# Optimization experiments

Measured on AMD Instinct MI355X. Metric: run time of the kernel, lower is better.

The kernel has to match this reference:

```python
import jax, jax.numpy as jnp
import numpy as np

N = 4096      # total_activities_num
D = 128       # feature dim
E = 1_000_000 # number of edges (events)
EPS = 1e-12


def setup_inputs() -> dict:
    key = jax.random.key(0)
    k1, k2, k3, k4, k5 = jax.random.split(key, 5)
    currents = jax.random.randint(k1, (E,), 0, N, dtype=jnp.int64)
    targets = jax.random.randint(k2, (E,), 0, N, dtype=jnp.int64)
    activities_features = jax.random.normal(k3, (N, D), dtype=jnp.float32)
    cases_features = jax.random.normal(k4, (E, D), dtype=jnp.float32)
    # Learned parameter W [N, N], kaiming_uniform fan_in relu -> U(-b, b), b = sqrt(6/fan_in)
    bound = float(np.sqrt(6.0 / N))
    W = jax.random.uniform(k5, (N, N), dtype=jnp.float32, minval=-bound, maxval=bound)
    return {
        "currents": currents,
        "targets": targets,
        "activities_features": activities_features,
        "cases_features": cases_features,
        "W": W,
    }


def reference(currents, targets, activities_features, cases_features, W):
    # Per-edge gather: h_emb, t_emb are [E, D]
    h_emb = activities_features[currents]
    t_emb = activities_features[targets]
    # dist = ||h + case - t||_2 per edge -> [E]
    diff = h_emb + cases_features - t_emb
    dist = jnp.sqrt(jnp.sum(diff * diff, axis=1))
    vals = jnp.exp(-dist)
    # Scatter-add into dense [N, N] attention input at (tail, head)
    att_input = jnp.zeros((N, N), dtype=activities_features.dtype)
    att_input = att_input.at[targets, currents].add(vals)
    # Row-normalize
    norm = jnp.sum(att_input, axis=1, keepdims=True)
    attention = att_input / (norm + EPS)
    # Dense GEMMs
    feat = W @ activities_features           # [N, D]
    h = attention @ feat + feat               # [N, D]
    return h
```

## Files before the change

kernel.cpp:

```cpp
#include <hip/hip_runtime.h>
#include <hip/hip_bf16.h>

typedef unsigned short u16;
typedef unsigned int   u32;

typedef __attribute__((ext_vector_type(8))) __bf16 bf16x8;
typedef __attribute__((ext_vector_type(4))) float  f32x4;
typedef __attribute__((ext_vector_type(4))) u32    u32x4;

#define NN 4096
#define DD 128
#define EPS 1e-12f

#define KS 4
#define BM 32
#define BK 128
#define KPER (NN / KS)
#define LDK 136

static __device__ __forceinline__ u16 f2bf(float f) {
    union { float f; u32 u; } v; v.f = f;
    u32 r = v.u + 0x7fffu + ((v.u >> 16) & 1u);
    return (u16)(r >> 16);
}
static __device__ __forceinline__ float bf2f(u16 u) {
    union { u32 i; float f; } v; v.i = (u32)u << 16; return v.f;
}

template <typename T>
static __device__ __forceinline__ auto bf2_atomic_add(T* p, T v, int)
    -> decltype(unsafeAtomicAdd(p, v), void()) {
    unsafeAtomicAdd(p, v);
}
template <typename T>
static __device__ __forceinline__ void bf2_atomic_add(T* p, T v, long) {
    u32* w = (u32*)p;
    union { u32 i; T h; } av; av.h = v;
    float alo = bf2f((u16)(av.i & 0xffff));
    float ahi = bf2f((u16)(av.i >> 16));
    u32 old = *w, assumed;
    do {
        assumed = old;
        float lo = bf2f((u16)(assumed & 0xffff)) + alo;
        float hi = bf2f((u16)(assumed >> 16)) + ahi;
        u32 nv = (u32)f2bf(lo) | ((u32)f2bf(hi) << 16);
        old = atomicCAS(w, assumed, nv);
    } while (old != assumed);
}

__global__ __launch_bounds__(256) void edge_kernel(
    const int* __restrict__ currents, const int* __restrict__ targets,
    const float* __restrict__ A, const float* __restrict__ cases,
    u16* __restrict__ att, int E)
{
    int e = blockIdx.x * 8 + (threadIdx.x >> 5);
    if (e >= E) return;
    int l = threadIdx.x & 31;
    int c = currents[e];
    int t = targets[e];
    f32x4 h = *(const f32x4*)(A + (size_t)c * DD + l * 4);
    f32x4 g = *(const f32x4*)(A + (size_t)t * DD + l * 4);
    f32x4 q = __builtin_nontemporal_load((const f32x4*)(cases + (size_t)e * DD + l * 4));
    float d0 = h.x + q.x - g.x;
    float d1 = h.y + q.y - g.y;
    float d2 = h.z + q.z - g.z;
    float d3 = h.w + q.w - g.w;
    float s = d0 * d0 + d1 * d1 + d2 * d2 + d3 * d3;
#pragma unroll
    for (int m = 16; m; m >>= 1) s += __shfl_xor(s, m, 64);
    if (l == 0) {
        float val = __expf(-__fsqrt_rn(s));
        u16 b = f2bf(val);
        size_t off = (size_t)t * NN + c;
        union { u32 i; __hip_bfloat162 h2; } pk;
        pk.i = (c & 1) ? ((u32)b << 16) : (u32)b;
        bf2_atomic_add((__hip_bfloat162*)(att + (off & ~(size_t)1)), pk.h2, 0);
    }
}

__global__ __launch_bounds__(256) void transpose_to_bf16(
    const float* __restrict__ in, u16* __restrict__ out)
{
    __shared__ __align__(16) u16 lds[128][40];
    const int k0 = blockIdx.x * 32;
    const int t = threadIdx.x;
#pragma unroll
    for (int i = 0; i < 4; ++i) {
        int f  = t + 256 * i;
        int kr = f >> 5;
        int n0 = (f & 31) * 4;
        float4 v = *(const float4*)(in + (size_t)(k0 + kr) * DD + n0);
        lds[n0 + 0][kr] = f2bf(v.x);
        lds[n0 + 1][kr] = f2bf(v.y);
        lds[n0 + 2][kr] = f2bf(v.z);
        lds[n0 + 3][kr] = f2bf(v.w);
    }
    __syncthreads();
    int n = t >> 1, h = t & 1;
    uint4 v0 = *(const uint4*)&lds[n][h * 16];
    uint4 v1 = *(const uint4*)&lds[n][h * 16 + 8];
    *(uint4*)(out + (size_t)n * NN + k0 + h * 16)     = v0;
    *(uint4*)(out + (size_t)n * NN + k0 + h * 16 + 8) = v1;
}

template<bool ROWSUM, bool ABF16>
__global__ __launch_bounds__(512, 4) void gemm_splitk(
    const void* __restrict__ AmatV,
    const u16*  __restrict__ BT,
    float* __restrict__ part,
    float* __restrict__ normsum)
{
    __shared__ __align__(16) u16 As[BM * LDK];
    __shared__ __align__(16) u16 Bs[DD * LDK];

    const int m0   = blockIdx.x * BM;
    const int ks   = blockIdx.y;
    const int kbeg = ks * KPER;
    const int t    = threadIdx.x;
    const int wave = t >> 6;
    const int lane = t & 63;
    const int quad = lane >> 4;
    const int l16  = lane & 15;

    const int ar = t >> 4;
    const int aq = t & 15;
    const int bn = t >> 2;
    const int bq = t & 3;

    const float* Apf = (const float*)AmatV + (size_t)(m0 + ar) * NN + kbeg + aq * 4;
    const u16*   Aph = (const u16*)AmatV   + (size_t)(m0 + ar) * NN + kbeg + aq * 8;
    const u16*   Bp  = BT + (size_t)bn * NN + kbeg + bq * 32;

    f32x4 va0, va1; u32x4 vah;
    if constexpr (ABF16) {
        vah = __builtin_nontemporal_load((const u32x4*)Aph);
    } else {
        va0 = __builtin_nontemporal_load((const f32x4*)Apf);
        va1 = __builtin_nontemporal_load((const f32x4*)(Apf + 64));
    }
    uint4 vb0 = *(const uint4*)(Bp);
    uint4 vb1 = *(const uint4*)(Bp + 8);
    uint4 vb2 = *(const uint4*)(Bp + 16);
    uint4 vb3 = *(const uint4*)(Bp + 24);

    f32x4 acc0 = {0.f, 0.f, 0.f, 0.f};
    f32x4 acc1 = {0.f, 0.f, 0.f, 0.f};
    float rsum = 0.f;

    for (int kk = 0; kk < KPER; kk += BK) {
        if constexpr (ABF16) {
            if (ROWSUM) {
#pragma unroll
            for (int j = 0; j < 4; ++j) {
                u32 w = vah[j];
                rsum += bf2f((u16)(w & 0xffff)) + bf2f((u16)(w >> 16));
            }
            }
            *(u32x4*)&As[ar * LDK + aq * 8] = vah;
        } else {
            if (ROWSUM) {
                rsum += (va0.x + va0.y) + (va0.z + va0.w)
                      + (va1.x + va1.y) + (va1.z + va1.w);
            }
            ushort4 u0, u1;
            u0.x = f2bf(va0.x); u0.y = f2bf(va0.y); u0.z = f2bf(va0.z); u0.w = f2bf(va0.w);
            u1.x = f2bf(va1.x); u1.y = f2bf(va1.y); u1.z = f2bf(va1.z); u1.w = f2bf(va1.w);
            *(ushort4*)&As[ar * LDK + aq * 4]      = u0;
            *(ushort4*)&As[ar * LDK + aq * 4 + 64] = u1;
        }
        *(uint4*)&Bs[bn * LDK + bq * 32]      = vb0;
        *(uint4*)&Bs[bn * LDK + bq * 32 + 8]  = vb1;
        *(uint4*)&Bs[bn * LDK + bq * 32 + 16] = vb2;
        *(uint4*)&Bs[bn * LDK + bq * 32 + 24] = vb3;
        __syncthreads();

        if (kk + BK < KPER) {
            int k1 = kk + BK;
            if constexpr (ABF16) {
                vah = __builtin_nontemporal_load((const u32x4*)(Aph + k1));
            } else {
                va0 = __builtin_nontemporal_load((const f32x4*)(Apf + k1));
                va1 = __builtin_nontemporal_load((const f32x4*)(Apf + k1 + 64));
            }
            vb0 = *(const uint4*)(Bp + k1);
            vb1 = *(const uint4*)(Bp + k1 + 8);
            vb2 = *(const uint4*)(Bp + k1 + 16);
            vb3 = *(const uint4*)(Bp + k1 + 24);
        }

#pragma unroll
        for (int k2 = 0; k2 < 4; ++k2) {
            bf16x8 a0 = *(const bf16x8*)&As[l16 * LDK + k2 * 32 + quad * 8];
            bf16x8 a1 = *(const bf16x8*)&As[(16 + l16) * LDK + k2 * 32 + quad * 8];
            bf16x8 b  = *(const bf16x8*)&Bs[(wave * 16 + l16) * LDK + k2 * 32 + quad * 8];
            acc0 = __builtin_amdgcn_mfma_f32_16x16x32_bf16(a0, b, acc0, 0, 0, 0);
            acc1 = __builtin_amdgcn_mfma_f32_16x16x32_bf16(a1, b, acc1, 0, 0, 0);
        }
        __syncthreads();
    }

    float* P = part + (size_t)ks * NN * DD;
#pragma unroll
    for (int r = 0; r < 4; ++r) {
        int row0 = m0 + quad * 4 + r;
        int col  = wave * 16 + l16;
        P[(size_t)row0 * DD + col]        = acc0[r];
        P[(size_t)(row0 + 16) * DD + col] = acc1[r];
    }

    if (ROWSUM) {
#pragma unroll
        for (int m = 8; m; m >>= 1) rsum += __shfl_xor(rsum, m, 64);
        if ((t & 15) == 0) atomicAdd(normsum + m0 + ar, rsum);
    }
}

__global__ __launch_bounds__(256) void combine_feat(
    const float* __restrict__ part, float* __restrict__ feat)
{
    int i = blockIdx.x * 256 + threadIdx.x;
    const float4* p = (const float4*)part;
    const int S = NN * DD / 4;
    float4 a = p[i], b = p[i + S], c = p[i + 2 * S], d = p[i + 3 * S];
    float4 s;
    s.x = (a.x + b.x) + (c.x + d.x);
    s.y = (a.y + b.y) + (c.y + d.y);
    s.z = (a.z + b.z) + (c.z + d.z);
    s.w = (a.w + b.w) + (c.w + d.w);
    ((float4*)feat)[i] = s;
}

__global__ __launch_bounds__(256) void combine_out(
    const float* __restrict__ part, const float* __restrict__ normsum,
    const float* __restrict__ feat, float* __restrict__ out)
{
    int i = blockIdx.x * 256 + threadIdx.x;
    int row = i >> 5;
    const float4* p = (const float4*)part;
    const int S = NN * DD / 4;
    float4 a = p[i], b = p[i + S], c = p[i + 2 * S], d = p[i + 3 * S];
    float sc = 1.0f / (normsum[row] + EPS);
    float4 f = ((const float4*)feat)[i];
    float4 s;
    s.x = ((a.x + b.x) + (c.x + d.x)) * sc + f.x;
    s.y = ((a.y + b.y) + (c.y + d.y)) * sc + f.y;
    s.z = ((a.z + b.z) + (c.z + d.z)) * sc + f.z;
    s.w = ((a.w + b.w) + (c.w + d.w)) * sc + f.w;
    ((float4*)out)[i] = s;
}

extern "C" void kernel_launch(void* const* d_in, const int* in_sizes, int n_in,
                              void* d_out, int out_size, void* d_ws, size_t ws_size,
                              hipStream_t stream)
{
    const int*   currents = (const int*)d_in[0];
    const int*   targets  = (const int*)d_in[1];
    const float* acts     = (const float*)d_in[2];
    const float* cases    = (const float*)d_in[3];
    const float* W        = (const float*)d_in[4];
    float*       out      = (float*)d_out;
    const int E = in_sizes[0];

    char* ws = (char*)d_ws;
    u16*   att     = (u16*)ws;
    float* part    = (float*)(ws + (size_t)NN * NN * 2);
    float* feat    = part + (size_t)KS * NN * DD;
    u16*   BT1     = (u16*)(feat + (size_t)NN * DD);
    u16*   BT2     = BT1 + (size_t)DD * NN;
    float* normsum = (float*)(BT2 + (size_t)DD * NN);

    hipMemsetAsync(att, 0, (size_t)NN * NN * 2, stream);
    hipMemsetAsync(normsum, 0, (size_t)NN * 4, stream);

    transpose_to_bf16<<<128, 256, 0, stream>>>(acts, BT1);

    edge_kernel<<<(E + 7) / 8, 256, 0, stream>>>(currents, targets, acts, cases,
                                                 att, E);

    gemm_splitk<false, false><<<dim3(NN / BM, KS), 512, 0, stream>>>(W, BT1, part, nullptr);
    combine_feat<<<NN * DD / 4 / 256, 256, 0, stream>>>(part, feat);

    transpose_to_bf16<<<128, 256, 0, stream>>>(feat, BT2);

    gemm_splitk<true, true><<<dim3(NN / BM, KS), 512, 0, stream>>>(att, BT2, part, normsum);
    combine_out<<<NN * DD / 4 / 256, 256, 0, stream>>>(part, normsum, feat, out);
}
```

Before: 197.5 us.

## Fuse edge scatter and W@A GEMM into one heterogeneous launch

Merges the edge scatter kernel and the first split-K GEMM (W @ activities) into a single kernel. The first 512 blocks do the GEMM and the remaining blocks process edges, 16 per 512-thread block. Because the two stages are independent, this lets the compute-bound GEMM overlap the memory- and atomic-bound edge work and saves one launch. The cost is that the edge blocks inherit the GEMM's LDS footprint and launch bounds, which may reduce their occupancy.

```diff
diff --git a/kernel.cpp b/kernel.cpp
--- a/kernel.cpp
+++ b/kernel.cpp
@@ -17,6 +17,7 @@
 #define BK 128
 #define KPER (NN / KS)
 #define LDK 136
+#define NGEMM (128 * KS)
 
 static __device__ __forceinline__ u16 f2bf(float f) {
     union { float f; u32 u; } v; v.f = f;
@@ -48,33 +49,109 @@
     } while (old != assumed);
 }
 
-__global__ __launch_bounds__(256) void edge_kernel(
-    const int* __restrict__ currents, const int* __restrict__ targets,
-    const float* __restrict__ A, const float* __restrict__ cases,
-    u16* __restrict__ att, int E)
-{
-    int e = blockIdx.x * 8 + (threadIdx.x >> 5);
-    if (e >= E) return;
-    int l = threadIdx.x & 31;
-    int c = currents[e];
-    int t = targets[e];
-    f32x4 h = *(const f32x4*)(A + (size_t)c * DD + l * 4);
-    f32x4 g = *(const f32x4*)(A + (size_t)t * DD + l * 4);
-    f32x4 q = __builtin_nontemporal_load((const f32x4*)(cases + (size_t)e * DD + l * 4));
-    float d0 = h.x + q.x - g.x;
-    float d1 = h.y + q.y - g.y;
-    float d2 = h.z + q.z - g.z;
-    float d3 = h.w + q.w - g.w;
-    float s = d0 * d0 + d1 * d1 + d2 * d2 + d3 * d3;
-#pragma unroll
-    for (int m = 16; m; m >>= 1) s += __shfl_xor(s, m, 64);
-    if (l == 0) {
-        float val = __expf(-__fsqrt_rn(s));
-        u16 b = f2bf(val);
-        size_t off = (size_t)t * NN + c;
-        union { u32 i; __hip_bfloat162 h2; } pk;
-        pk.i = (c & 1) ? ((u32)b << 16) : (u32)b;
-        bf2_atomic_add((__hip_bfloat162*)(att + (off & ~(size_t)1)), pk.h2, 0);
+__global__ __launch_bounds__(512, 4) void fused_edge_gemm(
+    const int*   __restrict__ currents, const int* __restrict__ targets,
+    const float* __restrict__ A,        const float* __restrict__ cases,
+    u16*         __restrict__ att,
+    const float* __restrict__ W,        const u16* __restrict__ BT,
+    float*       __restrict__ part,     int E)
+{
+    __shared__ __align__(16) u16 As[BM * LDK];
+    __shared__ __align__(16) u16 Bs[DD * LDK];
+    const int bid = blockIdx.x;
+
+    if (bid >= NGEMM) {
+        const int e = (bid - NGEMM) * 16 + ((int)threadIdx.x >> 5);
+        if (e >= E) return;
+        const int l = threadIdx.x & 31;
+        const int c = currents[e];
+        const int t = targets[e];
+        f32x4 h = *(const f32x4*)(A + (size_t)c * DD + l * 4);
+        f32x4 g = *(const f32x4*)(A + (size_t)t * DD + l * 4);
+        f32x4 q = __builtin_nontemporal_load(
+                      (const f32x4*)(cases + (size_t)e * DD + l * 4));
+        f32x4 d = h + q - g;
+        float s = d.x * d.x + d.y * d.y + d.z * d.z + d.w * d.w;
+#pragma unroll
+        for (int m = 16; m; m >>= 1) s += __shfl_xor(s, m, 64);
+        if (l == 0) {
+            float val = __expf(-__fsqrt_rn(s));
+            u16 b = f2bf(val);
+            size_t off = (size_t)t * NN + c;
+            union { u32 i; __hip_bfloat162 h2; } pk;
+            pk.i = (c & 1) ? ((u32)b << 16) : (u32)b;
+            bf2_atomic_add((__hip_bfloat162*)(att + (off & ~(size_t)1)), pk.h2, 0);
+        }
+        return;
+    }
+
+    const int m0   = (bid & 127) * BM;
+    const int ks   = bid >> 7;
+    const int kbeg = ks * KPER;
+    const int t    = threadIdx.x;
+    const int wave = t >> 6;
+    const int lane = t & 63;
+    const int quad = lane >> 4;
+    const int l16  = lane & 15;
+
+    const int ar = t >> 4;
+    const int aq = t & 15;
+    const int bn = t >> 2;
+    const int bq = t & 3;
+
+    const float* Ap = W  + (size_t)(m0 + ar) * NN + kbeg + aq * 4;
+    const u16*   Bp = BT + (size_t)bn * NN + kbeg + bq * 32;
+
+    f32x4 va0 = __builtin_nontemporal_load((const f32x4*)Ap);
+    f32x4 va1 = __builtin_nontemporal_load((const f32x4*)(Ap + 64));
+    uint4 vb0 = *(const uint4*)(Bp);
+    uint4 vb1 = *(const uint4*)(Bp + 8);
+    uint4 vb2 = *(const uint4*)(Bp + 16);
+    uint4 vb3 = *(const uint4*)(Bp + 24);
+
+    f32x4 acc0 = {0.f, 0.f, 0.f, 0.f};
+    f32x4 acc1 = {0.f, 0.f, 0.f, 0.f};
+
+    for (int kk = 0; kk < KPER; kk += BK) {
+        ushort4 u0, u1;
+        u0.x = f2bf(va0.x); u0.y = f2bf(va0.y); u0.z = f2bf(va0.z); u0.w = f2bf(va0.w);
+        u1.x = f2bf(va1.x); u1.y = f2bf(va1.y); u1.z = f2bf(va1.z); u1.w = f2bf(va1.w);
+        *(ushort4*)&As[ar * LDK + aq * 4]      = u0;
+        *(ushort4*)&As[ar * LDK + aq * 4 + 64] = u1;
+        *(uint4*)&Bs[bn * LDK + bq * 32]      = vb0;
+        *(uint4*)&Bs[bn * LDK + bq * 32 + 8]  = vb1;
+        *(uint4*)&Bs[bn * LDK + bq * 32 + 16] = vb2;
+        *(uint4*)&Bs[bn * LDK + bq * 32 + 24] = vb3;
+        __syncthreads();
+
+        if (kk + BK < KPER) {
+            int k1 = kk + BK;
+            va0 = __builtin_nontemporal_load((const f32x4*)(Ap + k1));
+            va1 = __builtin_nontemporal_load((const f32x4*)(Ap + k1 + 64));
+            vb0 = *(const uint4*)(Bp + k1);
+            vb1 = *(const uint4*)(Bp + k1 + 8);
+            vb2 = *(const uint4*)(Bp + k1 + 16);
+            vb3 = *(const uint4*)(Bp + k1 + 24);
+        }
+
+#pragma unroll
+        for (int k2 = 0; k2 < 4; ++k2) {
+            bf16x8 a0 = *(const bf16x8*)&As[l16 * LDK + k2 * 32 + quad * 8];
+            bf16x8 a1 = *(const bf16x8*)&As[(16 + l16) * LDK + k2 * 32 + quad * 8];
+            bf16x8 b  = *(const bf16x8*)&Bs[(wave * 16 + l16) * LDK + k2 * 32 + quad * 8];
+            acc0 = __builtin_amdgcn_mfma_f32_16x16x32_bf16(a0, b, acc0, 0, 0, 0);
+            acc1 = __builtin_amdgcn_mfma_f32_16x16x32_bf16(a1, b, acc1, 0, 0, 0);
+        }
+        __syncthreads();
+    }
+
+    float* P = part + (size_t)ks * NN * DD;
+#pragma unroll
+    for (int r = 0; r < 4; ++r) {
+        int row0 = m0 + quad * 4 + r;
+        int col  = wave * 16 + l16;
+        P[(size_t)row0 * DD + col]        = acc0[r];
+        P[(size_t)(row0 + 16) * DD + col] = acc1[r];
     }
 }
 
@@ -103,9 +180,8 @@
     *(uint4*)(out + (size_t)n * NN + k0 + h * 16 + 8) = v1;
 }
 
-template<bool ROWSUM, bool ABF16>
-__global__ __launch_bounds__(512, 4) void gemm_splitk(
-    const void* __restrict__ AmatV,
+__global__ __launch_bounds__(512, 4) void gemm2_att(
+    const u16*  __restrict__ Amat,
     const u16*  __restrict__ BT,
     float* __restrict__ part,
     float* __restrict__ normsum)
@@ -127,17 +203,10 @@
     const int bn = t >> 2;
     const int bq = t & 3;
 
-    const float* Apf = (const float*)AmatV + (size_t)(m0 + ar) * NN + kbeg + aq * 4;
-    const u16*   Aph = (const u16*)AmatV   + (size_t)(m0 + ar) * NN + kbeg + aq * 8;
-    const u16*   Bp  = BT + (size_t)bn * NN + kbeg + bq * 32;
-
-    f32x4 va0, va1; u32x4 vah;
-    if constexpr (ABF16) {
-        vah = __builtin_nontemporal_load((const u32x4*)Aph);
-    } else {
-        va0 = __builtin_nontemporal_load((const f32x4*)Apf);
-        va1 = __builtin_nontemporal_load((const f32x4*)(Apf + 64));
-    }
+    const u16* Aph = Amat + (size_t)(m0 + ar) * NN + kbeg + aq * 8;
+    const u16* Bp  = BT   + (size_t)bn * NN + kbeg + bq * 32;
+
+    u32x4 vah = __builtin_nontemporal_load((const u32x4*)Aph);
     uint4 vb0 = *(const uint4*)(Bp);
     uint4 vb1 = *(const uint4*)(Bp + 8);
     uint4 vb2 = *(const uint4*)(Bp + 16);
@@ -148,26 +217,12 @@
     float rsum = 0.f;
 
     for (int kk = 0; kk < KPER; kk += BK) {
-        if constexpr (ABF16) {
-            if (ROWSUM) {
-#pragma unroll
-            for (int j = 0; j < 4; ++j) {
-                u32 w = vah[j];
-                rsum += bf2f((u16)(w & 0xffff)) + bf2f((u16)(w >> 16));
-            }
-            }
-            *(u32x4*)&As[ar * LDK + aq * 8] = vah;
-        } else {
-            if (ROWSUM) {
-                rsum += (va0.x + va0.y) + (va0.z + va0.w)
-                      + (va1.x + va1.y) + (va1.z + va1.w);
-            }
-            ushort4 u0, u1;
-            u0.x = f2bf(va0.x); u0.y = f2bf(va0.y); u0.z = f2bf(va0.z); u0.w = f2bf(va0.w);
-            u1.x = f2bf(va1.x); u1.y = f2bf(va1.y); u1.z = f2bf(va1.z); u1.w = f2bf(va1.w);
-            *(ushort4*)&As[ar * LDK + aq * 4]      = u0;
-            *(ushort4*)&As[ar * LDK + aq * 4 + 64] = u1;
-        }
+#pragma unroll
+        for (int j = 0; j < 4; ++j) {
+            u32 w = vah[j];
+            rsum += bf2f((u16)(w & 0xffff)) + bf2f((u16)(w >> 16));
+        }
+        *(u32x4*)&As[ar * LDK + aq * 8] = vah;
         *(uint4*)&Bs[bn * LDK + bq * 32]      = vb0;
         *(uint4*)&Bs[bn * LDK + bq * 32 + 8]  = vb1;
         *(uint4*)&Bs[bn * LDK + bq * 32 + 16] = vb2;
@@ -176,12 +231,7 @@
 
         if (kk + BK < KPER) {
             int k1 = kk + BK;
-            if constexpr (ABF16) {
-                vah = __builtin_nontemporal_load((const u32x4*)(Aph + k1));
-            } else {
-                va0 = __builtin_nontemporal_load((const f32x4*)(Apf + k1));
-                va1 = __builtin_nontemporal_load((const f32x4*)(Apf + k1 + 64));
-            }
+            vah = __builtin_nontemporal_load((const u32x4*)(Aph + k1));
             vb0 = *(const uint4*)(Bp + k1);
             vb1 = *(const uint4*)(Bp + k1 + 8);
             vb2 = *(const uint4*)(Bp + k1 + 16);
@@ -208,11 +258,9 @@
         P[(size_t)(row0 + 16) * DD + col] = acc1[r];
     }
 
-    if (ROWSUM) {
-#pragma unroll
-        for (int m = 8; m; m >>= 1) rsum += __shfl_xor(rsum, m, 64);
-        if ((t & 15) == 0) atomicAdd(normsum + m0 + ar, rsum);
-    }
+#pragma unroll
+    for (int m = 8; m; m >>= 1) rsum += __shfl_xor(rsum, m, 64);
+    if ((t & 15) == 0) atomicAdd(normsum + m0 + ar, rsum);
 }
 
 __global__ __launch_bounds__(256) void combine_feat(
@@ -274,14 +322,14 @@
 
     transpose_to_bf16<<<128, 256, 0, stream>>>(acts, BT1);
 
-    edge_kernel<<<(E + 7) / 8, 256, 0, stream>>>(currents, targets, acts, cases,
-                                                 att, E);
-
-    gemm_splitk<false, false><<<dim3(NN / BM, KS), 512, 0, stream>>>(W, BT1, part, nullptr);
+    const int nEdgeBlk = (E + 15) / 16;
+    fused_edge_gemm<<<NGEMM + nEdgeBlk, 512, 0, stream>>>(
+        currents, targets, acts, cases, att, W, BT1, part, E);
+
     combine_feat<<<NN * DD / 4 / 256, 256, 0, stream>>>(part, feat);
 
     transpose_to_bf16<<<128, 256, 0, stream>>>(feat, BT2);
 
-    gemm_splitk<true, true><<<dim3(NN / BM, KS), 512, 0, stream>>>(att, BT2, part, normsum);
+    gemm2_att<<<dim3(NN / BM, KS), 512, 0, stream>>>(att, BT2, part, normsum);
     combine_out<<<NN * DD / 4 / 256, 256, 0, stream>>>(part, normsum, feat, out);
 }
```

After: 223.4 us. +13.1%, slower.

## Split edge kernel into value pass and separate dense atomic scatter pass

Applied to the files above, without the earlier changes.

Splits the per-edge work into two kernels. The first computes exp(-dist) into a float buffer with one write per edge. A second kernel, one thread per edge, does the CAS-based bf16 atomic scatter into the attention matrix, and the memset and scatter are moved to just before the second GEMM. The aim is to take the serialized atomics off the bandwidth-bound distance pass and run them at full thread parallelism, at the cost of an extra kernel launch and an extra read/write of the value array.

```diff
diff --git a/kernel.cpp b/kernel.cpp
--- a/kernel.cpp
+++ b/kernel.cpp
@@ -48,10 +48,10 @@
     } while (old != assumed);
 }
 
-__global__ __launch_bounds__(256) void edge_kernel(
+__global__ __launch_bounds__(256) void edge_val_kernel(
     const int* __restrict__ currents, const int* __restrict__ targets,
     const float* __restrict__ A, const float* __restrict__ cases,
-    u16* __restrict__ att, int E)
+    float* __restrict__ val, int E)
 {
     int e = blockIdx.x * 8 + (threadIdx.x >> 5);
     if (e >= E) return;
@@ -61,21 +61,26 @@
     f32x4 h = *(const f32x4*)(A + (size_t)c * DD + l * 4);
     f32x4 g = *(const f32x4*)(A + (size_t)t * DD + l * 4);
     f32x4 q = __builtin_nontemporal_load((const f32x4*)(cases + (size_t)e * DD + l * 4));
-    float d0 = h.x + q.x - g.x;
-    float d1 = h.y + q.y - g.y;
-    float d2 = h.z + q.z - g.z;
-    float d3 = h.w + q.w - g.w;
-    float s = d0 * d0 + d1 * d1 + d2 * d2 + d3 * d3;
+    f32x4 d = h + q - g;
+    float s = d.x * d.x + d.y * d.y + d.z * d.z + d.w * d.w;
 #pragma unroll
     for (int m = 16; m; m >>= 1) s += __shfl_xor(s, m, 64);
-    if (l == 0) {
-        float val = __expf(-__fsqrt_rn(s));
-        u16 b = f2bf(val);
-        size_t off = (size_t)t * NN + c;
-        union { u32 i; __hip_bfloat162 h2; } pk;
-        pk.i = (c & 1) ? ((u32)b << 16) : (u32)b;
-        bf2_atomic_add((__hip_bfloat162*)(att + (off & ~(size_t)1)), pk.h2, 0);
-    }
+    if (l == 0) val[e] = __expf(-__fsqrt_rn(s));
+}
+
+__global__ __launch_bounds__(256) void scatter_kernel(
+    const int* __restrict__ currents, const int* __restrict__ targets,
+    const float* __restrict__ val, u16* __restrict__ att, int E)
+{
+    int i = blockIdx.x * 256 + threadIdx.x;
+    if (i >= E) return;
+    int c = currents[i];
+    int t = targets[i];
+    u16 b = f2bf(val[i]);
+    size_t off = (size_t)t * NN + c;
+    union { u32 i_; __hip_bfloat162 h2; } pk;
+    pk.i_ = (c & 1) ? ((u32)b << 16) : (u32)b;
+    bf2_atomic_add((__hip_bfloat162*)(att + (off & ~(size_t)1)), pk.h2, 0);
 }
 
 __global__ __launch_bounds__(256) void transpose_to_bf16(
@@ -268,20 +273,25 @@
     u16*   BT1     = (u16*)(feat + (size_t)NN * DD);
     u16*   BT2     = BT1 + (size_t)DD * NN;
     float* normsum = (float*)(BT2 + (size_t)DD * NN);
-
-    hipMemsetAsync(att, 0, (size_t)NN * NN * 2, stream);
+    float* val     = normsum + NN;
+
     hipMemsetAsync(normsum, 0, (size_t)NN * 4, stream);
 
     transpose_to_bf16<<<128, 256, 0, stream>>>(acts, BT1);
 
-    edge_kernel<<<(E + 7) / 8, 256, 0, stream>>>(currents, targets, acts, cases,
-                                                 att, E);
+    edge_val_kernel<<<(E + 7) / 8, 256, 0, stream>>>(currents, targets, acts,
+                                                     cases, val, E);
 
     gemm_splitk<false, false><<<dim3(NN / BM, KS), 512, 0, stream>>>(W, BT1, part, nullptr);
     combine_feat<<<NN * DD / 4 / 256, 256, 0, stream>>>(part, feat);
 
     transpose_to_bf16<<<128, 256, 0, stream>>>(feat, BT2);
 
+    hipMemsetAsync(att, 0, (size_t)NN * NN * 2, stream);
+
+    scatter_kernel<<<(E + 255) / 256, 256, 0, stream>>>(currents, targets, val,
+                                                        att, E);
+
     gemm_splitk<true, true><<<dim3(NN / BM, KS), 512, 0, stream>>>(att, BT2, part, normsum);
     combine_out<<<NN * DD / 4 / 256, 256, 0, stream>>>(part, normsum, feat, out);
 }
```

After: 239.2 us. 21.1% more time.

## Fuse feat combine with bf16 transpose, deepen GEMM A prefetch, drop normsum atomics

Applied to the files above, without the earlier changes.

Merges the split-K combine of feat with the bf16 transpose into one kernel, removing one launch and a re-read of feat. The GEMM main loop is unrolled by two so the A tile is prefetched two steps ahead. Row sums now go into per-split slots that combine_out adds up, which removes the normsum memset and the atomics. The extra prefetch registers may reduce occupancy under the 512x4 launch bounds.

```diff
diff --git a/kernel.cpp b/kernel.cpp
--- a/kernel.cpp
+++ b/kernel.cpp
@@ -61,11 +61,8 @@
     f32x4 h = *(const f32x4*)(A + (size_t)c * DD + l * 4);
     f32x4 g = *(const f32x4*)(A + (size_t)t * DD + l * 4);
     f32x4 q = __builtin_nontemporal_load((const f32x4*)(cases + (size_t)e * DD + l * 4));
-    float d0 = h.x + q.x - g.x;
-    float d1 = h.y + q.y - g.y;
-    float d2 = h.z + q.z - g.z;
-    float d3 = h.w + q.w - g.w;
-    float s = d0 * d0 + d1 * d1 + d2 * d2 + d3 * d3;
+    f32x4 d = h + q - g;
+    float s = d.x * d.x + d.y * d.y + d.z * d.z + d.w * d.w;
 #pragma unroll
     for (int m = 16; m; m >>= 1) s += __shfl_xor(s, m, 64);
     if (l == 0) {
@@ -108,7 +105,7 @@
     const void* __restrict__ AmatV,
     const u16*  __restrict__ BT,
     float* __restrict__ part,
-    float* __restrict__ normsum)
+    float* __restrict__ rsum_part)
 {
     __shared__ __align__(16) u16 As[BM * LDK];
     __shared__ __align__(16) u16 Bs[DD * LDK];
@@ -131,12 +128,15 @@
     const u16*   Aph = (const u16*)AmatV   + (size_t)(m0 + ar) * NN + kbeg + aq * 8;
     const u16*   Bp  = BT + (size_t)bn * NN + kbeg + bq * 32;
 
-    f32x4 va0, va1; u32x4 vah;
+    f32x4 vaA0, vaA1, vaB0, vaB1; u32x4 vahA, vahB;
     if constexpr (ABF16) {
-        vah = __builtin_nontemporal_load((const u32x4*)Aph);
+        vahA = __builtin_nontemporal_load((const u32x4*)Aph);
+        vahB = __builtin_nontemporal_load((const u32x4*)(Aph + BK));
     } else {
-        va0 = __builtin_nontemporal_load((const f32x4*)Apf);
-        va1 = __builtin_nontemporal_load((const f32x4*)(Apf + 64));
+        vaA0 = __builtin_nontemporal_load((const f32x4*)Apf);
+        vaA1 = __builtin_nontemporal_load((const f32x4*)(Apf + 64));
+        vaB0 = __builtin_nontemporal_load((const f32x4*)(Apf + BK));
+        vaB1 = __builtin_nontemporal_load((const f32x4*)(Apf + BK + 64));
     }
     uint4 vb0 = *(const uint4*)(Bp);
     uint4 vb1 = *(const uint4*)(Bp + 8);
@@ -147,55 +147,84 @@
     f32x4 acc1 = {0.f, 0.f, 0.f, 0.f};
     float rsum = 0.f;
 
-    for (int kk = 0; kk < KPER; kk += BK) {
-        if constexpr (ABF16) {
-            if (ROWSUM) {
-#pragma unroll
-            for (int j = 0; j < 4; ++j) {
-                u32 w = vah[j];
-                rsum += bf2f((u16)(w & 0xffff)) + bf2f((u16)(w >> 16));
+#define STAGE_A_BF16(VAH)                                                   \
+    {                                                                       \
+        if (ROWSUM) {                                                       \
+            _Pragma("unroll")                                               \
+            for (int j = 0; j < 4; ++j) {                                   \
+                u32 w = (VAH)[j];                                           \
+                rsum += bf2f((u16)(w & 0xffff)) + bf2f((u16)(w >> 16));     \
+            }                                                               \
+        }                                                                   \
+        *(u32x4*)&As[ar * LDK + aq * 8] = (VAH);                            \
+    }
+#define STAGE_A_F32(V0, V1)                                                 \
+    {                                                                       \
+        if (ROWSUM) {                                                       \
+            rsum += ((V0).x + (V0).y) + ((V0).z + (V0).w)                   \
+                  + ((V1).x + (V1).y) + ((V1).z + (V1).w);                  \
+        }                                                                   \
+        ushort4 u0, u1;                                                     \
+        u0.x = f2bf((V0).x); u0.y = f2bf((V0).y);                           \
+        u0.z = f2bf((V0).z); u0.w = f2bf((V0).w);                           \
+        u1.x = f2bf((V1).x); u1.y = f2bf((V1).y);                           \
+        u1.z = f2bf((V1).z); u1.w = f2bf((V1).w);                           \
+        *(ushort4*)&As[ar * LDK + aq * 4]      = u0;                        \
+        *(ushort4*)&As[ar * LDK + aq * 4 + 64] = u1;                        \
+    }
+#define STAGE_B()                                                           \
+    {                                                                       \
+        *(uint4*)&Bs[bn * LDK + bq * 32]      = vb0;                        \
+        *(uint4*)&Bs[bn * LDK + bq * 32 + 8]  = vb1;                        \
+        *(uint4*)&Bs[bn * LDK + bq * 32 + 16] = vb2;                        \
+        *(uint4*)&Bs[bn * LDK + bq * 32 + 24] = vb3;                        \
+    }
+#define LOAD_B(KOFF)                                                        \
+    {                                                                       \
+        vb0 = *(const uint4*)(Bp + (KOFF));                                 \
+        vb1 = *(const uint4*)(Bp + (KOFF) + 8);                             \
+        vb2 = *(const uint4*)(Bp + (KOFF) + 16);                            \
+        vb3 = *(const uint4*)(Bp + (KOFF) + 24);                            \
+    }
+#define MFMA_PHASE()                                                        \
+    _Pragma("unroll")                                                       \
+    for (int k2 = 0; k2 < 4; ++k2) {                                        \
+        bf16x8 a0 = *(const bf16x8*)&As[l16 * LDK + k2 * 32 + quad * 8];    \
+        bf16x8 a1 = *(const bf16x8*)&As[(16 + l16) * LDK + k2 * 32 + quad * 8]; \
+        bf16x8 b  = *(const bf16x8*)&Bs[(wave * 16 + l16) * LDK + k2 * 32 + quad * 8]; \
+        acc0 = __builtin_amdgcn_mfma_f32_16x16x32_bf16(a0, b, acc0, 0, 0, 0); \
+        acc1 = __builtin_amdgcn_mfma_f32_16x16x32_bf16(a1, b, acc1, 0, 0, 0); \
+    }
+
+    for (int kk = 0; kk < KPER; kk += 2 * BK) {
+        if constexpr (ABF16) { STAGE_A_BF16(vahA); } else { STAGE_A_F32(vaA0, vaA1); }
+        STAGE_B();
+        __syncthreads();
+        if (kk + 2 * BK < KPER) {
+            if constexpr (ABF16) {
+                vahA = __builtin_nontemporal_load((const u32x4*)(Aph + kk + 2 * BK));
+            } else {
+                vaA0 = __builtin_nontemporal_load((const f32x4*)(Apf + kk + 2 * BK));
+                vaA1 = __builtin_nontemporal_load((const f32x4*)(Apf + kk + 2 * BK + 64));
             }
+        }
+        LOAD_B(kk + BK);
+        MFMA_PHASE();
+        __syncthreads();
+
+        if constexpr (ABF16) { STAGE_A_BF16(vahB); } else { STAGE_A_F32(vaB0, vaB1); }
+        STAGE_B();
+        __syncthreads();
+        if (kk + 3 * BK < KPER) {
+            if constexpr (ABF16) {
+                vahB = __builtin_nontemporal_load((const u32x4*)(Aph + kk + 3 * BK));
+            } else {
+                vaB0 = __builtin_nontemporal_load((const f32x4*)(Apf + kk + 3 * BK));
+                vaB1 = __builtin_nontemporal_load((const f32x4*)(Apf + kk + 3 * BK + 64));
             }
-            *(u32x4*)&As[ar * LDK + aq * 8] = vah;
-        } else {
-            if (ROWSUM) {
-                rsum += (va0.x + va0.y) + (va0.z + va0.w)
-                      + (va1.x + va1.y) + (va1.z + va1.w);
-            }
-            ushort4 u0, u1;
-            u0.x = f2bf(va0.x); u0.y = f2bf(va0.y); u0.z = f2bf(va0.z); u0.w = f2bf(va0.w);
-            u1.x = f2bf(va1.x); u1.y = f2bf(va1.y); u1.z = f2bf(va1.z); u1.w = f2bf(va1.w);
-            *(ushort4*)&As[ar * LDK + aq * 4]      = u0;
-            *(ushort4*)&As[ar * LDK + aq * 4 + 64] = u1;
         }
-        *(uint4*)&Bs[bn * LDK + bq * 32]      = vb0;
-        *(uint4*)&Bs[bn * LDK + bq * 32 + 8]  = vb1;
-        *(uint4*)&Bs[bn * LDK + bq * 32 + 16] = vb2;
-        *(uint4*)&Bs[bn * LDK + bq * 32 + 24] = vb3;
-        __syncthreads();
-
-        if (kk + BK < KPER) {
-            int k1 = kk + BK;
-            if constexpr (ABF16) {
-                vah = __builtin_nontemporal_load((const u32x4*)(Aph + k1));
-            } else {
-                va0 = __builtin_nontemporal_load((const f32x4*)(Apf + k1));
-                va1 = __builtin_nontemporal_load((const f32x4*)(Apf + k1 + 64));
-            }
-            vb0 = *(const uint4*)(Bp + k1);
-            vb1 = *(const uint4*)(Bp + k1 + 8);
-            vb2 = *(const uint4*)(Bp + k1 + 16);
-            vb3 = *(const uint4*)(Bp + k1 + 24);
-        }
-
-#pragma unroll
-        for (int k2 = 0; k2 < 4; ++k2) {
-            bf16x8 a0 = *(const bf16x8*)&As[l16 * LDK + k2 * 32 + quad * 8];
-            bf16x8 a1 = *(const bf16x8*)&As[(16 + l16) * LDK + k2 * 32 + quad * 8];
-            bf16x8 b  = *(const bf16x8*)&Bs[(wave * 16 + l16) * LDK + k2 * 32 + quad * 8];
-            acc0 = __builtin_amdgcn_mfma_f32_16x16x32_bf16(a0, b, acc0, 0, 0, 0);
-            acc1 = __builtin_amdgcn_mfma_f32_16x16x32_bf16(a1, b, acc1, 0, 0, 0);
-        }
+        if (kk + 2 * BK < KPER) LOAD_B(kk + 2 * BK);
+        MFMA_PHASE();
         __syncthreads();
     }
 
@@ -211,27 +240,52 @@
     if (ROWSUM) {
 #pragma unroll
         for (int m = 8; m; m >>= 1) rsum += __shfl_xor(rsum, m, 64);
-        if ((t & 15) == 0) atomicAdd(normsum + m0 + ar, rsum);
-    }
-}
-
-__global__ __launch_bounds__(256) void combine_feat(
-    const float* __restrict__ part, float* __restrict__ feat)
-{
-    int i = blockIdx.x * 256 + threadIdx.x;
-    const float4* p = (const float4*)part;
+        if ((t & 15) == 0) rsum_part[ks * NN + m0 + ar] = rsum;
+    }
+#undef STAGE_A_BF16
+#undef STAGE_A_F32
+#undef STAGE_B
+#undef LOAD_B
+#undef MFMA_PHASE
+}
+
+__global__ __launch_bounds__(256) void combine_feat_bt2(
+    const float* __restrict__ part, float* __restrict__ feat,
+    u16* __restrict__ BT2)
+{
+    __shared__ __align__(16) u16 lt[128][40];
+    const int b = blockIdx.x;
+    const int t = threadIdx.x;
     const int S = NN * DD / 4;
-    float4 a = p[i], b = p[i + S], c = p[i + 2 * S], d = p[i + 3 * S];
-    float4 s;
-    s.x = (a.x + b.x) + (c.x + d.x);
-    s.y = (a.y + b.y) + (c.y + d.y);
-    s.z = (a.z + b.z) + (c.z + d.z);
-    s.w = (a.w + b.w) + (c.w + d.w);
-    ((float4*)feat)[i] = s;
+    const int base = b * 1024;
+#pragma unroll
+    for (int it = 0; it < 4; ++it) {
+        int i = base + it * 256 + t;
+        const float4* p = (const float4*)part;
+        float4 a = p[i], b4 = p[i + S], c = p[i + 2 * S], d = p[i + 3 * S];
+        float4 s;
+        s.x = (a.x + b4.x) + (c.x + d.x);
+        s.y = (a.y + b4.y) + (c.y + d.y);
+        s.z = (a.z + b4.z) + (c.z + d.z);
+        s.w = (a.w + b4.w) + (c.w + d.w);
+        ((float4*)feat)[i] = s;
+        int lrow = it * 8 + (t >> 5);
+        int col0 = (i & 31) * 4;
+        lt[col0 + 0][lrow] = f2bf(s.x);
+        lt[col0 + 1][lrow] = f2bf(s.y);
+        lt[col0 + 2][lrow] = f2bf(s.z);
+        lt[col0 + 3][lrow] = f2bf(s.w);
+    }
+    __syncthreads();
+    int col = t >> 1, half = t & 1;
+    uint4 v0 = *(const uint4*)&lt[col][half * 16];
+    uint4 v1 = *(const uint4*)&lt[col][half * 16 + 8];
+    *(uint4*)(BT2 + (size_t)col * NN + b * 32 + half * 16)     = v0;
+    *(uint4*)(BT2 + (size_t)col * NN + b * 32 + half * 16 + 8) = v1;
 }
 
 __global__ __launch_bounds__(256) void combine_out(
-    const float* __restrict__ part, const float* __restrict__ normsum,
+    const float* __restrict__ part, const float* __restrict__ rsum_part,
     const float* __restrict__ feat, float* __restrict__ out)
 {
     int i = blockIdx.x * 256 + threadIdx.x;
@@ -239,7 +293,9 @@
     const float4* p = (const float4*)part;
     const int S = NN * DD / 4;
     float4 a = p[i], b = p[i + S], c = p[i + 2 * S], d = p[i + 3 * S];
-    float sc = 1.0f / (normsum[row] + EPS);
+    float ns = (rsum_part[row] + rsum_part[row + NN])
+             + (rsum_part[row + 2 * NN] + rsum_part[row + 3 * NN]);
+    float sc = 1.0f / (ns + EPS);
     float4 f = ((const float4*)feat)[i];
     float4 s;
     s.x = ((a.x + b.x) + (c.x + d.x)) * sc + f.x;
@@ -262,15 +318,14 @@
     const int E = in_sizes[0];
 
     char* ws = (char*)d_ws;
-    u16*   att     = (u16*)ws;
-    float* part    = (float*)(ws + (size_t)NN * NN * 2);
-    float* feat    = part + (size_t)KS * NN * DD;
-    u16*   BT1     = (u16*)(feat + (size_t)NN * DD);
-    u16*   BT2     = BT1 + (size_t)DD * NN;
-    float* normsum = (float*)(BT2 + (size_t)DD * NN);
+    u16*   att       = (u16*)ws;
+    float* part      = (float*)(ws + (size_t)NN * NN * 2);
+    float* feat      = part + (size_t)KS * NN * DD;
+    u16*   BT1       = (u16*)(feat + (size_t)NN * DD);
+    u16*   BT2       = BT1 + (size_t)DD * NN;
+    float* rsum_part = (float*)(BT2 + (size_t)DD * NN);
 
     hipMemsetAsync(att, 0, (size_t)NN * NN * 2, stream);
-    hipMemsetAsync(normsum, 0, (size_t)NN * 4, stream);
 
     transpose_to_bf16<<<128, 256, 0, stream>>>(acts, BT1);
 
@@ -278,10 +333,8 @@
                                                  att, E);
 
     gemm_splitk<false, false><<<dim3(NN / BM, KS), 512, 0, stream>>>(W, BT1, part, nullptr);
-    combine_feat<<<NN * DD / 4 / 256, 256, 0, stream>>>(part, feat);
-
-    transpose_to_bf16<<<128, 256, 0, stream>>>(feat, BT2);
-
-    gemm_splitk<true, true><<<dim3(NN / BM, KS), 512, 0, stream>>>(att, BT2, part, normsum);
-    combine_out<<<NN * DD / 4 / 256, 256, 0, stream>>>(part, normsum, feat, out);
-}
+    combine_feat_bt2<<<128, 256, 0, stream>>>(part, feat, BT2);
+
+    gemm_splitk<true, true><<<dim3(NN / BM, KS), 512, 0, stream>>>(att, BT2, part, rsum_part);
+    combine_out<<<NN * DD / 4 / 256, 256, 0, stream>>>(part, rsum_part, feat, out);
+}
```

After: 189.9 us. 1.04x faster.
